# Kernel tuning notes

Hardware: AMD Instinct MI355X
Metric: run time of the kernel (lower is better)

Reference implementation:

```python
import jax, jax.numpy as jnp
import numpy as np

B, T, V, H, D = 32, 2048, 8, 5, 128  # batch, time, n_vars, history_len, d_model


def _init_w(k, shape, fan_in):
    return jax.random.normal(k, shape, jnp.float32) * (1.0 / np.sqrt(fan_in))


def setup_inputs() -> dict:
    key = jax.random.key(0)
    ks = jax.random.split(key, 8)
    return {
        "x": jax.random.normal(ks[0], (B, T, V), jnp.float32),
        "history": jax.random.normal(ks[1], (B, T, V * H), jnp.float32),
        # context_encoder: Linear(V*H -> D), ReLU, Linear(D -> V*V)
        "ce_w1": _init_w(ks[2], (D, V * H), V * H),
        "ce_b1": jnp.zeros((D,), jnp.float32),
        "ce_w2": _init_w(ks[3], (V * V, D), D),
        "ce_b2": jnp.zeros((V * V,), jnp.float32),
        # projector: Linear(1 -> D), ReLU, Linear(D -> D)
        "p_w1": _init_w(ks[4], (D, 1), 1),
        "p_b1": jnp.zeros((D,), jnp.float32),
        "p_w2": _init_w(ks[5], (D, D), D),
        "p_b2": jnp.zeros((D,), jnp.float32),
        # Wq / Wk: Linear(D -> D, bias=False)
        "wq": _init_w(ks[6], (D, D), D),
        "wk": _init_w(ks[7], (D, D), D),
    }


def reference(x, history, ce_w1, ce_b1, ce_w2, ce_b2,
              p_w1, p_b1, p_w2, p_b2, wq, wk):
    b, t, v = x.shape
    d = wq.shape[0]
    # gate: sigmoid(context_encoder(history)) reshaped to [B,T,V,V]
    h = jax.nn.relu(history @ ce_w1.T + ce_b1)                      # [B,T,D]
    gate = jax.nn.sigmoid((h @ ce_w2.T + ce_b2).reshape(b, t, v, v))
    # projector applied per scalar: Linear(1->D) == x[...,None] * w1_col + b1
    feat = jax.nn.relu(x[..., None] * p_w1[:, 0] + p_b1)            # [B,T,V,D]
    feat = feat @ p_w2.T + p_b2                                     # [B,T,V,D]
    q = feat @ wq.T                                                 # [B,T,V,D]
    k = feat @ wk.T                                                 # [B,T,V,D]
    scores = jnp.einsum('btid,btjd->btij', q, k) / jnp.sqrt(jnp.asarray(d, feat.dtype))
    A = jnp.tanh(scores) * gate                                     # [B,T,V,V]
    pred = jnp.einsum('btij,btj->bti', A, x)                        # [B,T,V]
    return pred, A
```

## Files before the change

### kernel.cpp

```cpp
#include <hip/hip_runtime.h>
#include <hip/hip_bf16.h>
#include <stdint.h>

#define Dm 128
#define BTOT (32 * 2048)

typedef short s16x8 __attribute__((ext_vector_type(8)));
typedef float f32x4 __attribute__((ext_vector_type(4)));

__device__ float g_Wq[Dm * Dm];
__device__ float g_Wk[Dm * Dm];
__device__ float g_bq[Dm], g_bk[Dm];
__device__ float g_u[Dm], g_w[Dm], g_c[1];
__device__ __align__(16) unsigned short g_AllFrag[32768];

__device__ __forceinline__ float fast_sigmoid(float x) { return 1.0f / (1.0f + __expf(-x)); }
__device__ __forceinline__ float fast_tanh(float x) { return 1.0f - 2.0f / (__expf(2.0f * x) + 1.0f); }

__device__ __forceinline__ unsigned short f2bf(float f) {
    unsigned u = __float_as_uint(f);
    u += 0x7fffu + ((u >> 16) & 1u);
    return (unsigned short)(u >> 16);
}

__device__ __forceinline__ unsigned pk2(float lo, float hi) {
    unsigned short ua = __builtin_bit_cast(unsigned short, (__bf16)lo);
    unsigned short ub = __builtin_bit_cast(unsigned short, (__bf16)hi);
    return (unsigned)ua | ((unsigned)ub << 16);
}

__device__ __forceinline__ s16x8 mk8(unsigned a, unsigned b, unsigned c, unsigned d) {
    union { unsigned u[4]; s16x8 v; } t;
    t.u[0] = a; t.u[1] = b; t.u[2] = c; t.u[3] = d;
    return t.v;
}

__device__ __forceinline__ void compute_rpf(float xv, int g,
                                            const float* __restrict__ p_w1,
                                            const float* __restrict__ p_b1,
                                            s16x8* rpf, float& sj_out) {
    float sj = 0.f;
#pragma unroll
    for (int kc = 0; kc < 4; ++kc) {
        unsigned wds[4];
#pragma unroll
        for (int jh = 0; jh < 2; ++jh) {
            const int d4 = kc * 32 + 4 * g + 16 * jh;
            f32x4 w1v = *(const f32x4*)&p_w1[d4];
            f32x4 b1v = *(const f32x4*)&p_b1[d4];
            f32x4 wvv = *(const f32x4*)&g_w[d4];
            float v[4];
#pragma unroll
            for (int jj = 0; jj < 4; ++jj) {
                float val = fmaxf(fmaf(xv, w1v[jj], b1v[jj]), 0.f);
                sj = fmaf(wvv[jj], val, sj);
                v[jj] = val;
            }
            wds[jh * 2 + 0] = pk2(v[0], v[1]);
            wds[jh * 2 + 1] = pk2(v[2], v[3]);
        }
        rpf[kc] = mk8(wds[0], wds[1], wds[2], wds[3]);
    }
    sj += __shfl_xor(sj, 16);
    sj += __shfl_xor(sj, 32);
    sj_out = sj;
}

__global__ __launch_bounds__(128) void k_pre1(const float* __restrict__ wq,
                                              const float* __restrict__ wk,
                                              const float* __restrict__ pw2,
                                              const float* __restrict__ pb2,
                                              const float* __restrict__ ce_w1,
                                              const float* __restrict__ ce_b1,
                                              const float* __restrict__ ce_w2) {
    const int b = blockIdx.x, t = threadIdx.x;
    if (b < 128) {
        const int g = b, d = t;
        float aq0 = 0.f, aq1 = 0.f, ak0 = 0.f, ak1 = 0.f;
#pragma unroll 8
        for (int f2 = 0; f2 < 64; ++f2) {
            float wqa = wq[g * Dm + 2 * f2], wqb = wq[g * Dm + 2 * f2 + 1];
            float wka = wk[g * Dm + 2 * f2], wkb = wk[g * Dm + 2 * f2 + 1];
            float pva = pw2[(2 * f2) * Dm + d], pvb = pw2[(2 * f2 + 1) * Dm + d];
            aq0 = fmaf(wqa, pva, aq0);
            aq1 = fmaf(wqb, pvb, aq1);
            ak0 = fmaf(wka, pva, ak0);
            ak1 = fmaf(wkb, pvb, ak1);
        }
        g_Wq[g * Dm + d] = aq0 + aq1;
        g_Wk[g * Dm + d] = ak0 + ak1;
        if (d == 0) {
            float bq0 = 0.f, bq1 = 0.f, bk0 = 0.f, bk1 = 0.f;
#pragma unroll 8
            for (int f2 = 0; f2 < 64; ++f2) {
                float pba = pb2[2 * f2], pbb = pb2[2 * f2 + 1];
                bq0 = fmaf(wq[g * Dm + 2 * f2], pba, bq0);
                bq1 = fmaf(wq[g * Dm + 2 * f2 + 1], pbb, bq1);
                bk0 = fmaf(wk[g * Dm + 2 * f2], pba, bk0);
                bk1 = fmaf(wk[g * Dm + 2 * f2 + 1], pbb, bk1);
            }
            g_bq[g] = bq0 + bq1;
            g_bk[g] = bk0 + bk1;
        }
    } else if (b < 136) {
        const int s = (b - 128) * 128 + t;
        const int l = s & 63, slot = s >> 6;
        const int rt = slot >> 1, kc = slot & 1;
        const int row = rt * 16 + (l & 15), gg = l >> 4;
#pragma unroll
        for (int j = 0; j < 8; ++j) {
            int k = kc * 32 + 4 * gg + (j & 3) + 16 * (j >> 2);
            float v = (k < 40) ? ce_w1[row * 40 + k] : ((k == 40) ? ce_b1[row] : 0.f);
            g_AllFrag[24576 + s * 8 + j] = f2bf(v);
        }
    } else {
        const int s = (b - 136) * 128 + t;
        const int l = s & 63, slot = s >> 6;
        const int rt2 = slot >> 2, kc = slot & 3;
        const int o = rt2 * 16 + (l & 15), gg = l >> 4;
#pragma unroll
        for (int j = 0; j < 8; ++j) {
            int k = kc * 32 + 4 * gg + (j & 3) + 16 * (j >> 2);
            g_AllFrag[16384 + s * 8 + j] = f2bf(ce_w2[o * Dm + k]);
        }
    }
}

__global__ __launch_bounds__(128) void k_pre2() {
    const int b = blockIdx.x, tid = threadIdx.x;
    if (b < 128) {
        const int slot = b >> 2, jj = b & 3;
        const int kc = slot & 3, rt = slot >> 2;
        const int l = tid & 63, jh = tid >> 6;
        const int row = rt * 16 + (l & 15), g = l >> 4;
        const int e = kc * 32 + 4 * g + jj + 16 * jh;
        float a0 = 0.f, a1 = 0.f;
#pragma unroll 8
        for (int g2 = 0; g2 < 64; ++g2) {
            a0 = fmaf(g_Wq[(2 * g2) * Dm + row], g_Wk[(2 * g2) * Dm + e], a0);
            a1 = fmaf(g_Wq[(2 * g2 + 1) * Dm + row], g_Wk[(2 * g2 + 1) * Dm + e], a1);
        }
        g_AllFrag[(slot * 64 + l) * 8 + 4 * jh + jj] = f2bf(a0 + a1);
    } else {
        const int d = tid;
        float u0 = 0.f, u1 = 0.f, w0 = 0.f, w1 = 0.f;
#pragma unroll 8
        for (int g2 = 0; g2 < 64; ++g2) {
            u0 = fmaf(g_Wq[(2 * g2) * Dm + d], g_bk[2 * g2], u0);
            u1 = fmaf(g_Wq[(2 * g2 + 1) * Dm + d], g_bk[2 * g2 + 1], u1);
            w0 = fmaf(g_Wk[(2 * g2) * Dm + d], g_bq[2 * g2], w0);
            w1 = fmaf(g_Wk[(2 * g2 + 1) * Dm + d], g_bq[2 * g2 + 1], w1);
        }
        g_u[d] = u0 + u1;
        g_w[d] = w0 + w1;
        if (d == 0) {
            float c0 = 0.f, c1 = 0.f;
#pragma unroll 8
            for (int g2 = 0; g2 < 64; ++g2) {
                c0 = fmaf(g_bq[2 * g2], g_bk[2 * g2], c0);
                c1 = fmaf(g_bq[2 * g2 + 1], g_bk[2 * g2 + 1], c1);
            }
            g_c[0] = c0 + c1;
        }
    }
}

__global__ __launch_bounds__(256) void k_fused(const float* __restrict__ x,
                                               const float* __restrict__ hist,
                                               const float* __restrict__ ce_b2,
                                               const float* __restrict__ p_w1,
                                               const float* __restrict__ p_b1,
                                               float* __restrict__ pred_out,
                                               float* __restrict__ A_out) {
    __shared__ __align__(16) unsigned short lds_m[16384];
    __shared__ __align__(16) unsigned short lds_hB[2048];
    __shared__ __align__(16) char lds_hg[16 * 41 * 4];
    float* lds_hist = (float*)lds_hg;
    unsigned* lds_gateP = (unsigned*)lds_hg;

    const int tid = threadIdx.x;
    const int wv = tid >> 6;
    const int l = tid & 63;
    const int g = l >> 4, c16 = l & 15;
    const long base = (long)blockIdx.x * 16;

    {
        const char* gsrc = (const char*)g_AllFrag + (size_t)wv * 8192 + (size_t)l * 16;
        char* ldst = (char*)lds_m + wv * 8192;
#pragma unroll
        for (int q = 0; q < 8; ++q)
            __builtin_amdgcn_global_load_lds(
                (const __attribute__((address_space(1))) unsigned int*)(gsrc + q * 1024),
                (__attribute__((address_space(3))) unsigned int*)(ldst + q * 1024), 16, 0, 0);
    }
    {
        const float* hsrc = hist + base * 40;
        lds_hist[(tid / 40) * 41 + (tid % 40)] = hsrc[tid];
        int i2 = tid + 256;
        lds_hist[(i2 / 40) * 41 + (i2 % 40)] = hsrc[i2];
        if (tid < 128) {
            int i3 = tid + 512;
            lds_hist[(i3 / 40) * 41 + (i3 % 40)] = hsrc[i3];
        }
    }
    s16x8 w1fA[2][2];
#pragma unroll
    for (int rr = 0; rr < 2; ++rr)
#pragma unroll
        for (int kc = 0; kc < 2; ++kc)
            w1fA[rr][kc] = *(const s16x8*)&g_AllFrag[24576 + (((2 * wv + rr) * 2 + kc) * 64 + l) * 8];
    s16x8 w2fA[4];
#pragma unroll
    for (int kc = 0; kc < 4; ++kc)
        w2fA[kc] = *(const s16x8*)&g_AllFrag[16384 + ((wv * 4 + kc) * 64 + l) * 8];
    f32x4 b2v = *(const f32x4*)&ce_b2[16 * wv + 4 * g];

    const int np = c16 >> 3, i_me = c16 & 7;
    const float xv0 = x[(base + wv * 4 + 0 + np) * 8 + i_me];
    const float xv1 = x[(base + wv * 4 + 2 + np) * 8 + i_me];
    s16x8 rpf0[4], rpf1[4];
    float sj0, sj1;
    compute_rpf(xv0, g, p_w1, p_b1, rpf0, sj0);
    compute_rpf(xv1, g, p_w1, p_b1, rpf1, sj1);
    const float cc = g_c[0];

    __syncthreads();

    const float* hl = lds_hist + c16 * 41;
    s16x8 histB[2];
    histB[0] = mk8(pk2(hl[4 * g + 0], hl[4 * g + 1]),
                   pk2(hl[4 * g + 2], hl[4 * g + 3]),
                   pk2(hl[16 + 4 * g + 0], hl[16 + 4 * g + 1]),
                   pk2(hl[16 + 4 * g + 2], hl[16 + 4 * g + 3]));
    {
        float v[4];
#pragma unroll
        for (int jj = 0; jj < 4; ++jj) {
            int k = 32 + 4 * g + jj;
            int kk = (k < 40) ? k : 0;
            float t = hl[kk];
            t = (k < 40) ? t : 0.f;
            v[jj] = (k == 40) ? 1.f : t;
        }
        histB[1] = mk8(pk2(v[0], v[1]), pk2(v[2], v[3]), 0u, 0u);
    }

#pragma unroll
    for (int rr = 0; rr < 2; ++rr) {
        f32x4 hC = (f32x4){0.f, 0.f, 0.f, 0.f};
        hC = __builtin_amdgcn_mfma_f32_16x16x32_bf16(w1fA[rr][0], histB[0], hC, 0, 0, 0);
        hC = __builtin_amdgcn_mfma_f32_16x16x32_bf16(w1fA[rr][1], histB[1], hC, 0, 0, 0);
        unsigned* dst = (unsigned*)&lds_hB[(wv * 64 + l) * 8 + rr * 4];
        dst[0] = pk2(fmaxf(hC[0], 0.f), fmaxf(hC[1], 0.f));
        dst[1] = pk2(fmaxf(hC[2], 0.f), fmaxf(hC[3], 0.f));
    }

    __syncthreads();

    {
        s16x8 gB[4];
#pragma unroll
        for (int kc = 0; kc < 4; ++kc)
            gB[kc] = *(const s16x8*)&lds_hB[(kc * 64 + l) * 8];
        f32x4 gC = b2v;
#pragma unroll
        for (int kc = 0; kc < 4; ++kc)
            gC = __builtin_amdgcn_mfma_f32_16x16x32_bf16(w2fA[kc], gB[kc], gC, 0, 0, 0);
        unsigned* gp = lds_gateP + c16 * 33 + 8 * wv + 2 * g;
        gp[0] = pk2(fast_sigmoid(gC[0]), fast_sigmoid(gC[1]));
        gp[1] = pk2(fast_sigmoid(gC[2]), fast_sigmoid(gC[3]));
    }

    f32x4 Sacc0 = (f32x4){0.f, 0.f, 0.f, 0.f};
    f32x4 Sacc1 = (f32x4){0.f, 0.f, 0.f, 0.f};
#pragma unroll
    for (int rt = 0; rt < 4; ++rt) {
        const int r0 = 2 * rt, r1 = 2 * rt + 1;
        f32x4 uv0 = *(const f32x4*)&g_u[16 * r0 + 4 * g];
        f32x4 uv1 = *(const f32x4*)&g_u[16 * r1 + 4 * g];
        f32x4 Ya0 = uv0, Yb0 = uv1;
        f32x4 Ya1 = uv0, Yb1 = uv1;
#pragma unroll
        for (int kc = 0; kc < 4; ++kc) {
            s16x8 af0 = *(const s16x8*)&lds_m[((r0 * 4 + kc) * 64 + l) * 8];
            s16x8 af1 = *(const s16x8*)&lds_m[((r1 * 4 + kc) * 64 + l) * 8];
            Ya0 = __builtin_amdgcn_mfma_f32_16x16x32_bf16(af0, rpf0[kc], Ya0, 0, 0, 0);
            Ya1 = __builtin_amdgcn_mfma_f32_16x16x32_bf16(af0, rpf1[kc], Ya1, 0, 0, 0);
            Yb0 = __builtin_amdgcn_mfma_f32_16x16x32_bf16(af1, rpf0[kc], Yb0, 0, 0, 0);
            Yb1 = __builtin_amdgcn_mfma_f32_16x16x32_bf16(af1, rpf1[kc], Yb1, 0, 0, 0);
        }
        s16x8 yf0 = mk8(pk2(Ya0[0], Ya0[1]), pk2(Ya0[2], Ya0[3]),
                        pk2(Yb0[0], Yb0[1]), pk2(Yb0[2], Yb0[3]));
        s16x8 yf1 = mk8(pk2(Ya1[0], Ya1[1]), pk2(Ya1[2], Ya1[3]),
                        pk2(Yb1[0], Yb1[1]), pk2(Yb1[2], Yb1[3]));
        Sacc0 = __builtin_amdgcn_mfma_f32_16x16x32_bf16(rpf0[rt], yf0, Sacc0, 0, 0, 0);
        Sacc1 = __builtin_amdgcn_mfma_f32_16x16x32_bf16(rpf1[rt], yf1, Sacc1, 0, 0, 0);
    }

    __syncthreads();

    const int jv = c16 & 7;
    const bool diag = ((g >> 1) == np);
    auto do_epi = [&](const f32x4& Sacc, float sjv, float xvv, int s) {
        const int bp = wv * 4 + s * 2 + np;
        const long bt = base + bp;
        float Av[4], pr[4];
#pragma unroll
        for (int q = 0; q < 4; ++q) {
            float sc = (Sacc[q] + sjv + cc) * 0.08838834764831845f;
            unsigned wg = lds_gateP[bp * 33 + (4 * (g & 1) + q) * 4 + (jv >> 1)];
            float gv = __uint_as_float((jv & 1) ? (wg & 0xffff0000u) : (wg << 16));
            Av[q] = fast_tanh(sc) * gv;
            pr[q] = Av[q] * xvv;
            pr[q] += __shfl_xor(pr[q], 1);
            pr[q] += __shfl_xor(pr[q], 2);
            pr[q] += __shfl_xor(pr[q], 4);
        }
        if (diag) {
            float* Ap = A_out + bt * 64 + jv;
#pragma unroll
            for (int q = 0; q < 4; ++q) Ap[((g & 1) * 4 + q) * 8] = Av[q];
            if (jv == 0) {
                float* Pp = pred_out + bt * 8 + (g & 1) * 4;
#pragma unroll
                for (int q = 0; q < 4; ++q) Pp[q] = pr[q];
            }
        }
    };
    do_epi(Sacc0, sj0, xv0, 0);
    do_epi(Sacc1, sj1, xv1, 1);
}

extern "C" void kernel_launch(void* const* d_in, const int* in_sizes, int n_in,
                              void* d_out, int out_size, void* d_ws, size_t ws_size,
                              hipStream_t stream) {
    const float* x = (const float*)d_in[0];
    const float* hist = (const float*)d_in[1];
    const float* ce_w1 = (const float*)d_in[2];
    const float* ce_b1 = (const float*)d_in[3];
    const float* ce_w2 = (const float*)d_in[4];
    const float* ce_b2 = (const float*)d_in[5];
    const float* p_w1 = (const float*)d_in[6];
    const float* p_b1 = (const float*)d_in[7];
    const float* p_w2 = (const float*)d_in[8];
    const float* p_b2 = (const float*)d_in[9];
    const float* wq = (const float*)d_in[10];
    const float* wk = (const float*)d_in[11];

    float* pred_out = (float*)d_out;
    float* A_out = pred_out + (size_t)BTOT * 8;

    k_pre1<<<144, 128, 0, stream>>>(wq, wk, p_w2, p_b2, ce_w1, ce_b1, ce_w2);
    k_pre2<<<129, 128, 0, stream>>>();
    k_fused<<<BTOT / 16, 256, 0, stream>>>(x, hist, ce_b2, p_w1, p_b1, pred_out, A_out);
}
```

Measured before the change: 64.15 us.

## Switch per-timestep score computation to 32x32x16 MFMA with repacked M fragments

Replaces the 16x16x32 bf16 MFMA formulation of the bilinear score path with 32x32x16 MFMAs, packing four timesteps' 8 variables into 32 columns so each wave computes all its scores in one accumulator. The precomputed Wq^T Wk fragment layout in k_pre2 and the feature fragment construction are reshaped to match the 32-wide layout. This removes the redundant off-diagonal work of the earlier paired-16-column scheme and the duplicated rpf computation. The risks are higher register pressure from the 16-wide accumulators, and a fragment layout that must exactly match the MFMA operand mapping for results to stay correct.

```diff
diff --git a/kernel.cpp b/kernel.cpp
--- a/kernel.cpp
+++ b/kernel.cpp
@@ -7,6 +7,7 @@
 
 typedef short s16x8 __attribute__((ext_vector_type(8)));
 typedef float f32x4 __attribute__((ext_vector_type(4)));
+typedef float f32x16 __attribute__((ext_vector_type(16)));
 
 __device__ float g_Wq[Dm * Dm];
 __device__ float g_Wk[Dm * Dm];
@@ -35,17 +36,20 @@
     return t.v;
 }
 
-__device__ __forceinline__ void compute_rpf(float xv, int g,
-                                            const float* __restrict__ p_w1,
-                                            const float* __restrict__ p_b1,
-                                            s16x8* rpf, float& sj_out) {
+#define MFMA16(a, b, c) __builtin_amdgcn_mfma_f32_16x16x32_bf16(a, b, c, 0, 0, 0)
+#define MFMA32(a, b, c) __builtin_amdgcn_mfma_f32_32x32x16_bf16(a, b, c, 0, 0, 0)
+
+__device__ __forceinline__ void compute_rpf32(float xv, int hi,
+                                              const float* __restrict__ p_w1,
+                                              const float* __restrict__ p_b1,
+                                              s16x8* rpf, float& sj_out) {
     float sj = 0.f;
 #pragma unroll
-    for (int kc = 0; kc < 4; ++kc) {
+    for (int c = 0; c < 8; ++c) {
         unsigned wds[4];
 #pragma unroll
         for (int jh = 0; jh < 2; ++jh) {
-            const int d4 = kc * 32 + 4 * g + 16 * jh;
+            const int d4 = c * 16 + jh * 8 + 4 * hi;
             f32x4 w1v = *(const f32x4*)&p_w1[d4];
             f32x4 b1v = *(const f32x4*)&p_b1[d4];
             f32x4 wvv = *(const f32x4*)&g_w[d4];
@@ -59,9 +63,8 @@
             wds[jh * 2 + 0] = pk2(v[0], v[1]);
             wds[jh * 2 + 1] = pk2(v[2], v[3]);
         }
-        rpf[kc] = mk8(wds[0], wds[1], wds[2], wds[3]);
-    }
-    sj += __shfl_xor(sj, 16);
+        rpf[c] = mk8(wds[0], wds[1], wds[2], wds[3]);
+    }
     sj += __shfl_xor(sj, 32);
     sj_out = sj;
 }
@@ -129,18 +132,18 @@
 __global__ __launch_bounds__(128) void k_pre2() {
     const int b = blockIdx.x, tid = threadIdx.x;
     if (b < 128) {
-        const int slot = b >> 2, jj = b & 3;
-        const int kc = slot & 3, rt = slot >> 2;
-        const int l = tid & 63, jh = tid >> 6;
-        const int row = rt * 16 + (l & 15), g = l >> 4;
-        const int e = kc * 32 + 4 * g + jj + 16 * jh;
+        const int slot = b >> 2, jpair = b & 3;
+        const int l = tid & 63, j = jpair * 2 + (tid >> 6);
+        const int rt = slot >> 3, c = slot & 7;
+        const int row = 32 * rt + (l & 31);
+        const int dcol = 16 * c + (j & 3) + 8 * (j >> 2) + 4 * (l >> 5);
         float a0 = 0.f, a1 = 0.f;
 #pragma unroll 8
         for (int g2 = 0; g2 < 64; ++g2) {
-            a0 = fmaf(g_Wq[(2 * g2) * Dm + row], g_Wk[(2 * g2) * Dm + e], a0);
-            a1 = fmaf(g_Wq[(2 * g2 + 1) * Dm + row], g_Wk[(2 * g2 + 1) * Dm + e], a1);
-        }
-        g_AllFrag[(slot * 64 + l) * 8 + 4 * jh + jj] = f2bf(a0 + a1);
+            a0 = fmaf(g_Wq[(2 * g2) * Dm + row], g_Wk[(2 * g2) * Dm + dcol], a0);
+            a1 = fmaf(g_Wq[(2 * g2 + 1) * Dm + row], g_Wk[(2 * g2 + 1) * Dm + dcol], a1);
+        }
+        g_AllFrag[(slot * 64 + l) * 8 + j] = f2bf(a0 + a1);
     } else {
         const int d = tid;
         float u0 = 0.f, u1 = 0.f, w0 = 0.f, w1 = 0.f;
@@ -182,6 +185,7 @@
     const int wv = tid >> 6;
     const int l = tid & 63;
     const int g = l >> 4, c16 = l & 15;
+    const int c31 = l & 31, hi = l >> 5;
     const long base = (long)blockIdx.x * 16;
 
     {
@@ -215,13 +219,11 @@
         w2fA[kc] = *(const s16x8*)&g_AllFrag[16384 + ((wv * 4 + kc) * 64 + l) * 8];
     f32x4 b2v = *(const f32x4*)&ce_b2[16 * wv + 4 * g];
 
-    const int np = c16 >> 3, i_me = c16 & 7;
-    const float xv0 = x[(base + wv * 4 + 0 + np) * 8 + i_me];
-    const float xv1 = x[(base + wv * 4 + 2 + np) * 8 + i_me];
-    s16x8 rpf0[4], rpf1[4];
-    float sj0, sj1;
-    compute_rpf(xv0, g, p_w1, p_b1, rpf0, sj0);
-    compute_rpf(xv1, g, p_w1, p_b1, rpf1, sj1);
+    const int pj = c31 >> 3, jv = c31 & 7;
+    const float xv = x[(base + wv * 4 + pj) * 8 + jv];
+    s16x8 rpf[8];
+    float sj;
+    compute_rpf32(xv, hi, p_w1, p_b1, rpf, sj);
     const float cc = g_c[0];
 
     __syncthreads();
@@ -248,8 +250,8 @@
 #pragma unroll
     for (int rr = 0; rr < 2; ++rr) {
         f32x4 hC = (f32x4){0.f, 0.f, 0.f, 0.f};
-        hC = __builtin_amdgcn_mfma_f32_16x16x32_bf16(w1fA[rr][0], histB[0], hC, 0, 0, 0);
-        hC = __builtin_amdgcn_mfma_f32_16x16x32_bf16(w1fA[rr][1], histB[1], hC, 0, 0, 0);
+        hC = MFMA16(w1fA[rr][0], histB[0], hC);
+        hC = MFMA16(w1fA[rr][1], histB[1], hC);
         unsigned* dst = (unsigned*)&lds_hB[(wv * 64 + l) * 8 + rr * 4];
         dst[0] = pk2(fmaxf(hC[0], 0.f), fmaxf(hC[1], 0.f));
         dst[1] = pk2(fmaxf(hC[2], 0.f), fmaxf(hC[3], 0.f));
@@ -265,70 +267,76 @@
         f32x4 gC = b2v;
 #pragma unroll
         for (int kc = 0; kc < 4; ++kc)
-            gC = __builtin_amdgcn_mfma_f32_16x16x32_bf16(w2fA[kc], gB[kc], gC, 0, 0, 0);
+            gC = MFMA16(w2fA[kc], gB[kc], gC);
         unsigned* gp = lds_gateP + c16 * 33 + 8 * wv + 2 * g;
         gp[0] = pk2(fast_sigmoid(gC[0]), fast_sigmoid(gC[1]));
         gp[1] = pk2(fast_sigmoid(gC[2]), fast_sigmoid(gC[3]));
     }
 
-    f32x4 Sacc0 = (f32x4){0.f, 0.f, 0.f, 0.f};
-    f32x4 Sacc1 = (f32x4){0.f, 0.f, 0.f, 0.f};
-#pragma unroll
-    for (int rt = 0; rt < 4; ++rt) {
-        const int r0 = 2 * rt, r1 = 2 * rt + 1;
-        f32x4 uv0 = *(const f32x4*)&g_u[16 * r0 + 4 * g];
-        f32x4 uv1 = *(const f32x4*)&g_u[16 * r1 + 4 * g];
-        f32x4 Ya0 = uv0, Yb0 = uv1;
-        f32x4 Ya1 = uv0, Yb1 = uv1;
-#pragma unroll
-        for (int kc = 0; kc < 4; ++kc) {
-            s16x8 af0 = *(const s16x8*)&lds_m[((r0 * 4 + kc) * 64 + l) * 8];
-            s16x8 af1 = *(const s16x8*)&lds_m[((r1 * 4 + kc) * 64 + l) * 8];
-            Ya0 = __builtin_amdgcn_mfma_f32_16x16x32_bf16(af0, rpf0[kc], Ya0, 0, 0, 0);
-            Ya1 = __builtin_amdgcn_mfma_f32_16x16x32_bf16(af0, rpf1[kc], Ya1, 0, 0, 0);
-            Yb0 = __builtin_amdgcn_mfma_f32_16x16x32_bf16(af1, rpf0[kc], Yb0, 0, 0, 0);
-            Yb1 = __builtin_amdgcn_mfma_f32_16x16x32_bf16(af1, rpf1[kc], Yb1, 0, 0, 0);
-        }
-        s16x8 yf0 = mk8(pk2(Ya0[0], Ya0[1]), pk2(Ya0[2], Ya0[3]),
-                        pk2(Yb0[0], Yb0[1]), pk2(Yb0[2], Yb0[3]));
-        s16x8 yf1 = mk8(pk2(Ya1[0], Ya1[1]), pk2(Ya1[2], Ya1[3]),
-                        pk2(Yb1[0], Yb1[1]), pk2(Yb1[2], Yb1[3]));
-        Sacc0 = __builtin_amdgcn_mfma_f32_16x16x32_bf16(rpf0[rt], yf0, Sacc0, 0, 0, 0);
-        Sacc1 = __builtin_amdgcn_mfma_f32_16x16x32_bf16(rpf1[rt], yf1, Sacc1, 0, 0, 0);
+    f32x16 Sacc;
+#pragma unroll
+    for (int w = 0; w < 16; ++w) Sacc[w] = 0.f;
+#pragma unroll
+    for (int rtp = 0; rtp < 2; ++rtp) {
+        const int rt0 = 2 * rtp, rt1 = 2 * rtp + 1;
+        f32x16 Y0, Y1;
+#pragma unroll
+        for (int bq = 0; bq < 4; ++bq) {
+            f32x4 u0 = *(const f32x4*)&g_u[rt0 * 32 + 8 * bq + 4 * hi];
+            f32x4 u1 = *(const f32x4*)&g_u[rt1 * 32 + 8 * bq + 4 * hi];
+#pragma unroll
+            for (int w = 0; w < 4; ++w) {
+                Y0[4 * bq + w] = u0[w];
+                Y1[4 * bq + w] = u1[w];
+            }
+        }
+#pragma unroll
+        for (int c = 0; c < 8; ++c) {
+            s16x8 af0 = *(const s16x8*)&lds_m[((rt0 * 8 + c) * 64 + l) * 8];
+            s16x8 af1 = *(const s16x8*)&lds_m[((rt1 * 8 + c) * 64 + l) * 8];
+            Y0 = MFMA32(af0, rpf[c], Y0);
+            Y1 = MFMA32(af1, rpf[c], Y1);
+        }
+#pragma unroll
+        for (int p = 0; p < 2; ++p) {
+            s16x8 yf0 = mk8(pk2(Y0[8 * p + 0], Y0[8 * p + 1]), pk2(Y0[8 * p + 2], Y0[8 * p + 3]),
+                            pk2(Y0[8 * p + 4], Y0[8 * p + 5]), pk2(Y0[8 * p + 6], Y0[8 * p + 7]));
+            Sacc = MFMA32(rpf[rt0 * 2 + p], yf0, Sacc);
+            s16x8 yf1 = mk8(pk2(Y1[8 * p + 0], Y1[8 * p + 1]), pk2(Y1[8 * p + 2], Y1[8 * p + 3]),
+                            pk2(Y1[8 * p + 4], Y1[8 * p + 5]), pk2(Y1[8 * p + 6], Y1[8 * p + 7]));
+            Sacc = MFMA32(rpf[rt1 * 2 + p], yf1, Sacc);
+        }
     }
 
     __syncthreads();
 
-    const int jv = c16 & 7;
-    const bool diag = ((g >> 1) == np);
-    auto do_epi = [&](const f32x4& Sacc, float sjv, float xvv, int s) {
-        const int bp = wv * 4 + s * 2 + np;
-        const long bt = base + bp;
-        float Av[4], pr[4];
-#pragma unroll
-        for (int q = 0; q < 4; ++q) {
-            float sc = (Sacc[q] + sjv + cc) * 0.08838834764831845f;
-            unsigned wg = lds_gateP[bp * 33 + (4 * (g & 1) + q) * 4 + (jv >> 1)];
-            float gv = __uint_as_float((jv & 1) ? (wg & 0xffff0000u) : (wg << 16));
-            Av[q] = fast_tanh(sc) * gv;
-            pr[q] = Av[q] * xvv;
-            pr[q] += __shfl_xor(pr[q], 1);
-            pr[q] += __shfl_xor(pr[q], 2);
-            pr[q] += __shfl_xor(pr[q], 4);
-        }
-        if (diag) {
-            float* Ap = A_out + bt * 64 + jv;
-#pragma unroll
-            for (int q = 0; q < 4; ++q) Ap[((g & 1) * 4 + q) * 8] = Av[q];
-            if (jv == 0) {
-                float* Pp = pred_out + bt * 8 + (g & 1) * 4;
-#pragma unroll
-                for (int q = 0; q < 4; ++q) Pp[q] = pr[q];
-            }
-        }
-    };
-    do_epi(Sacc0, sj0, xv0, 0);
-    do_epi(Sacc1, sj1, xv1, 1);
+    const long bt = base + wv * 4 + pj;
+    float Av[4], pr[4];
+#pragma unroll
+    for (int q = 0; q < 4; ++q) {
+        float s01 = (pj & 1) ? Sacc[4 + q] : Sacc[q];
+        float s23 = (pj & 1) ? Sacc[12 + q] : Sacc[8 + q];
+        float sv = (pj & 2) ? s23 : s01;
+        float sc = (sv + sj + cc) * 0.08838834764831845f;
+        const int ri = q + 4 * hi;
+        unsigned wg = lds_gateP[(wv * 4 + pj) * 33 + ri * 4 + (jv >> 1)];
+        float gv = __uint_as_float((jv & 1) ? (wg & 0xffff0000u) : (wg << 16));
+        Av[q] = fast_tanh(sc) * gv;
+        pr[q] = Av[q] * xv;
+        pr[q] += __shfl_xor(pr[q], 1);
+        pr[q] += __shfl_xor(pr[q], 2);
+        pr[q] += __shfl_xor(pr[q], 4);
+    }
+    {
+        float* Ap = A_out + bt * 64 + jv;
+#pragma unroll
+        for (int q = 0; q < 4; ++q) Ap[(q + 4 * hi) * 8] = Av[q];
+        if (jv == 0) {
+            float* Pp = pred_out + bt * 8 + 4 * hi;
+#pragma unroll
+            for (int q = 0; q < 4; ++q) Pp[q] = pr[q];
+        }
+    }
 }
 
 extern "C" void kernel_launch(void* const* d_in, const int* in_sizes, int n_in,
```

Result: slower. 73.42 us (+14.4%).
